# Kernel tuning notes

Hardware: AMD Instinct MI355X
Metric: run time of the kernel (lower is better)

Reference implementation:

```python
import jax, jax.numpy as jnp
import numpy as np
from jax import lax

# dims
B, N, D, H, K, NS = 16, 4096, 64, 128, 32, 1024  # clouds, pts/cloud, feat, hidden, max neighbors, fps samples
R = 0.2  # radius


def _fps(pos, n_s):
    """Farthest point sampling on one cloud. pos: [N,3] -> idx [n_s] int32."""
    n = pos.shape[0]

    def step(carry, _):
        dist, last = carry
        d = jnp.sum((pos - pos[last]) ** 2, axis=-1)
        dist = jnp.minimum(dist, d)
        nxt = jnp.argmax(dist).astype(jnp.int32)
        return (dist, nxt), last

    init = (jnp.full((n,), 1e10, pos.dtype), jnp.int32(0))
    _, idx = lax.scan(step, init, None, length=n_s)
    return idx


def setup_inputs() -> dict:
    key = jax.random.key(0)
    ks = jax.random.split(key, 6)
    s1 = 1.0 / np.sqrt(D + 1)
    s2 = 1.0 / np.sqrt(H)
    s3 = 1.0 / np.sqrt(D + H)
    return {
        "x": jax.random.normal(ks[0], (B, N, D), jnp.float32),
        "pos": jax.random.uniform(ks[1], (B, N, 3), jnp.float32),
        "W1": jax.random.normal(ks[2], (D + 1, H), jnp.float32) * s1,
        "b1": jnp.zeros((H,), jnp.float32),
        "W2": jax.random.normal(ks[3], (H, 3), jnp.float32) * s2,
        "b2": jnp.zeros((3,), jnp.float32),
        "W3": jax.random.normal(ks[4], (D + H, H), jnp.float32) * s3,
        "b3": jnp.zeros((H,), jnp.float32),
    }


def reference(x, pos, W1, b1, W2, b2, W3, b3):
    # 1) FPS downsample per cloud -> centers
    idx = jax.vmap(lambda p: _fps(p, NS))(pos)                    # [B,NS]
    pos_s = jax.vmap(lambda p, i: p[i])(pos, idx)                 # [B,NS,3]

    # 2) radius neighbor search: nearest-K within R (<= max_num_neighbors=32)
    d2 = jnp.sum((pos_s[:, :, None, :] - pos[:, None, :, :]) ** 2, axis=-1)  # [B,NS,N]
    masked = jnp.where(d2 <= R * R, d2, jnp.inf)
    neg, nbr = lax.top_k(-masked, K)                              # nearest K
    valid = (-neg) <= R * R                                       # [B,NS,K]

    # 3) gather neighbor features/positions
    x_j = jax.vmap(lambda a, i: a[i])(x, nbr)                     # [B,NS,K,D]
    pos_j = jax.vmap(lambda a, i: a[i])(pos, nbr)                 # [B,NS,K,3]
    diff = pos_j - pos_s[:, :, None, :]                           # pos_j - pos_i
    d2sel = jnp.sum(diff ** 2, axis=-1)
    dist = jnp.where(d2sel > 0, jnp.sqrt(jnp.where(d2sel > 0, d2sel, 1.0)), 0.0)

    # 4) message MLPs
    feat = jnp.concatenate([x_j, dist[..., None]], axis=-1)       # [B,NS,K,D+1]
    emb = jax.nn.relu(feat @ W1 + b1)                             # nn_msg_x
    pw = emb @ W2 + b2                                            # nn_msg_pos
    pmsg = diff * pw

    # 5) masked aggregate: sum for x, mean for pos
    m = valid[..., None].astype(emb.dtype)
    aggr_x = jnp.sum(emb * m, axis=2)                             # [B,NS,H]
    cnt = jnp.maximum(jnp.sum(m, axis=2), 1.0)                    # [B,NS,1]
    aggr_pos = jnp.sum(pmsg * m, axis=2) / cnt                    # [B,NS,3]

    # 6) update
    x_d = jax.vmap(lambda a, i: a[i])(x, idx)                     # [B,NS,D]
    out_x = jax.nn.relu(jnp.concatenate([x_d, aggr_x], axis=-1) @ W3 + b3)
    out_pos = pos_s + aggr_pos
    return out_x, out_pos, idx
```

## Files before the change

### kernel.cpp

```cpp
#include <hip/hip_runtime.h>
#include <math.h>

#define B_ 16
#define N_ 4096
#define D_ 64
#define H_ 128
#define K_ 32
#define NS_ 1024
#define R2_ 0.04f
#define CAP_ 1024

typedef short short8 __attribute__((ext_vector_type(8)));
typedef float f32x4 __attribute__((ext_vector_type(4)));

static __device__ __forceinline__ short f2bf(float f) {
    unsigned u = __float_as_uint(f);
    unsigned r = (u + 0x7FFFu + ((u >> 16) & 1u)) >> 16;
    return (short)r;
}

template<int CTRL, int RM>
static __device__ __forceinline__ unsigned dppmov(unsigned v) {
    return (unsigned)__builtin_amdgcn_update_dpp((int)v, (int)v, CTRL, RM, 0xF, false);
}

#define DPP_FMAX_STEP(CTRL, RM)                                           \
    {                                                                     \
        float n = __uint_as_float(dppmov<CTRL, RM>(__float_as_uint(wm))); \
        wm = fmaxf(wm, n);                                                \
    }

#define DPP_UMIN_STEP(CTRL, RM)                                           \
    {                                                                     \
        unsigned n = dppmov<CTRL, RM>(cand);                              \
        cand = n < cand ? n : cand;                                       \
    }

#define DPP_UMIN_STEP_V(var, CTRL, RM)                                    \
    {                                                                     \
        unsigned n = dppmov<CTRL, RM>(var);                               \
        var = n < var ? n : var;                                          \
    }

__global__ __launch_bounds__(256, 1) void mega_kernel(
    const float* __restrict__ pos, const float* __restrict__ x,
    const float* __restrict__ W1, const float* __restrict__ b1,
    const float* __restrict__ W2, const float* __restrict__ b2,
    const float* __restrict__ W3, const float* __restrict__ b3,
    int* ticket, int* progress, int* idx_i, float* pos_s,
    float* out_x, float* out_pos, float* idx_f)
{
    __shared__ __align__(16) char smem[66048];
    __shared__ int srole;
    const int t = threadIdx.x;
    if (t == 0) srole = atomicAdd(ticket, 1);
    __syncthreads();
    const int my = srole;
    const int wv = t >> 6;
    const int lane = t & 63;

    if (my < B_) {
        float4* lpos4 = (float4*)smem;
        unsigned long long (*skey)[4] = (unsigned long long (*)[4])(smem + 65536);
        float4 (*scoord)[4] = (float4 (*)[4])(smem + 65536 + 64);
        const int b = my;
        const float* posb = pos + (size_t)b * N_ * 3;
        for (int p = t; p < N_; p += 256)
            lpos4[p] = make_float4(posb[3 * p + 0], posb[3 * p + 1], posb[3 * p + 2], 0.f);
        __syncthreads();

        float px[16], py[16], pz[16], dist[16];
#pragma unroll
        for (int j = 0; j < 16; ++j) {
            float4 v = lpos4[t + 256 * j];
            px[j] = v.x; py[j] = v.y; pz[j] = v.z;
            dist[j] = 1e10f;
        }
        unsigned curidx = 0;
        float4 c0 = lpos4[0];
        float ccx = c0.x, ccy = c0.y, ccz = c0.z;

        for (int ns = 0; ns < NS_; ++ns) {
            if (t == 0) {
                idx_i[b * NS_ + ns] = (int)curidx;
                idx_f[b * NS_ + ns] = (float)curidx;
                pos_s[(b * NS_ + ns) * 3 + 0] = ccx;
                pos_s[(b * NS_ + ns) * 3 + 1] = ccy;
                pos_s[(b * NS_ + ns) * 3 + 2] = ccz;
            }
            float bv = -1.f; int bj = 0;
#pragma unroll
            for (int j = 0; j < 16; ++j) {
                float dx = __fsub_rn(px[j], ccx);
                float dy = __fsub_rn(py[j], ccy);
                float dz = __fsub_rn(pz[j], ccz);
                float d2 = __fadd_rn(__fadd_rn(__fmul_rn(dx, dx), __fmul_rn(dy, dy)), __fmul_rn(dz, dz));
                float dn = fminf(dist[j], d2);
                dist[j] = dn;
                bool g = dn > bv;
                bv = g ? dn : bv;
                bj = g ? j : bj;
            }
            float wm = bv;
            DPP_FMAX_STEP(0x111, 0xF)
            DPP_FMAX_STEP(0x112, 0xF)
            DPP_FMAX_STEP(0x114, 0xF)
            DPP_FMAX_STEP(0x118, 0xF)
            DPP_FMAX_STEP(0x142, 0xA)
            DPP_FMAX_STEP(0x143, 0xC)
            const float wavemax = __uint_as_float(
                (unsigned)__builtin_amdgcn_readlane((int)__float_as_uint(wm), 63));
            const unsigned pidx = (unsigned)t + ((unsigned)bj << 8);
            const unsigned long long mask = __ballot(bv == wavemax);
            unsigned widx;
            if (__popcll(mask) == 1) {
                const int wl = __ffsll((long long)mask) - 1;
                widx = (unsigned)__builtin_amdgcn_readlane((int)pidx, wl);
            } else {
                unsigned cand = (bv == wavemax) ? pidx : 0xFFFFFFFFu;
                DPP_UMIN_STEP(0x111, 0xF)
                DPP_UMIN_STEP(0x112, 0xF)
                DPP_UMIN_STEP(0x114, 0xF)
                DPP_UMIN_STEP(0x118, 0xF)
                DPP_UMIN_STEP(0x142, 0xA)
                DPP_UMIN_STEP(0x143, 0xC)
                widx = (unsigned)__builtin_amdgcn_readlane((int)cand, 63);
            }
            float4 wc = lpos4[widx];
            if (lane == 0) {
                skey[ns & 1][wv] = (((unsigned long long)__float_as_uint(wavemax)) << 32)
                                 | (unsigned long long)(0xFFFFFFFFu - widx);
                scoord[ns & 1][wv] = wc;
            }
            __syncthreads();
            {
                unsigned sid = (unsigned)(lane & 3);
                unsigned long long skv = skey[ns & 1][sid];
                float4 scv = scoord[ns & 1][sid];
                unsigned kh2 = (unsigned)(skv >> 32), kl2 = (unsigned)skv;
#define SLOT_STEP(CTRL)                                                        \
                {                                                              \
                    unsigned nh = dppmov<CTRL, 0xF>(kh2);                      \
                    unsigned nl = dppmov<CTRL, 0xF>(kl2);                      \
                    unsigned nsid = dppmov<CTRL, 0xF>(sid);                    \
                    unsigned long long nk = (((unsigned long long)nh) << 32) | nl; \
                    unsigned long long ok = (((unsigned long long)kh2) << 32) | kl2;\
                    if (nk > ok) { kh2 = nh; kl2 = nl; sid = nsid; }           \
                }
                SLOT_STEP(0x101)
                SLOT_STEP(0x102)
#undef SLOT_STEP
                const int slotwin = __builtin_amdgcn_readfirstlane((int)sid);
                curidx = 0xFFFFFFFFu - (unsigned)__builtin_amdgcn_readfirstlane((int)kl2);
                ccx = __uint_as_float((unsigned)__builtin_amdgcn_readlane(
                          (int)__float_as_uint(scv.x), slotwin));
                ccy = __uint_as_float((unsigned)__builtin_amdgcn_readlane(
                          (int)__float_as_uint(scv.y), slotwin));
                ccz = __uint_as_float((unsigned)__builtin_amdgcn_readlane(
                          (int)__float_as_uint(scv.z), slotwin));
            }
            if (((ns & 63) == 63) && t == 0) {
                __threadfence();
                __hip_atomic_store(progress + b, ns + 1,
                                   __ATOMIC_RELEASE, __HIP_MEMORY_SCOPE_AGENT);
            }
        }
        return;
    }

    const int wt = my - B_;
    const int b = wt & 15;
    const int c = wt >> 4;
    const int s0 = b * NS_ + c * 16;
    const int quad = lane >> 4, cl = lane & 15;
    unsigned long long* ckw = (unsigned long long*)smem + (size_t)wv * CAP_;
    char* wbp = smem + 32768 + wv * 5120;
    float* rows = (float*)(smem + 53248);

    short8 bfrag[8][2];
    float b1v[8], w1dv[8], w2v0[8], w2v1[8], w2v2[8];
#pragma unroll
    for (int Nt = 0; Nt < 8; ++Nt) {
        const int h = Nt * 16 + cl;
#pragma unroll
        for (int ks = 0; ks < 2; ++ks) {
            short8 f;
#pragma unroll
            for (int jj = 0; jj < 8; ++jj)
                f[jj] = f2bf(W1[(ks * 32 + quad * 8 + jj) * H_ + h]);
            bfrag[Nt][ks] = f;
        }
        b1v[Nt] = b1[h];
        w1dv[Nt] = W1[64 * H_ + h];
        w2v0[Nt] = W2[h * 3 + 0];
        w2v1[Nt] = W2[h * 3 + 1];
        w2v2[Nt] = W2[h * 3 + 2];
    }
    const float b20 = b2[0], b21 = b2[1], b22 = b2[2];

    if (t == 0) {
        const int need = c * 16 + 16;
        while (__hip_atomic_load(progress + b, __ATOMIC_ACQUIRE,
                                 __HIP_MEMORY_SCOPE_AGENT) < need)
            __builtin_amdgcn_s_sleep(8);
    }
    __syncthreads();
    __threadfence();

    const volatile float* psv = pos_s;
    const volatile int*   iiv = idx_i;
    const float* posb = pos + (size_t)b * N_ * 3;
    const int kkg = lane >> 1, half = lane & 1;

    for (int i = 0; i < 4; ++i) {
        const int s = s0 + wv * 4 + i;
        const int sl = wv * 4 + i;
        const float cx = psv[s * 3 + 0], cy = psv[s * 3 + 1], cz = psv[s * 3 + 2];
        int m = 0;
        for (int base = 0; base < N_; base += 64) {
            int p = base + lane;
            float dx = __fsub_rn(posb[3 * p + 0], cx);
            float dy = __fsub_rn(posb[3 * p + 1], cy);
            float dz = __fsub_rn(posb[3 * p + 2], cz);
            float d2 = __fadd_rn(__fadd_rn(__fmul_rn(dx, dx), __fmul_rn(dy, dy)), __fmul_rn(dz, dz));
            bool in = (d2 <= R2_);
            unsigned long long msk = __ballot(in);
            int before = __popcll(msk & ((1ull << lane) - 1ull));
            int slot = m + before;
            if (in && slot < CAP_)
                ckw[slot] = ((unsigned long long)__float_as_uint(d2) << 32) | (unsigned)p;
            m += __popcll(msk);
        }
        if (m > CAP_) m = CAP_;
        __asm__ volatile("s_waitcnt lgkmcnt(0)" ::: "memory");
        const int kcnt = m < K_ ? m : K_;
        int nidx = -1;
        if (m <= 256) {
            unsigned long long kr[4];
#pragma unroll
            for (int r = 0; r < 4; ++r) {
                int q = r * 64 + lane;
                unsigned long long v = ckw[q & (CAP_ - 1)];
                kr[r] = (q < m) ? v : ~0ull;
            }
            unsigned chosen = 0;
            for (int k = 0; k < kcnt; ++k) {
                unsigned long long localk = ~0ull; int br = -1;
#pragma unroll
                for (int r = 0; r < 4; ++r) {
                    bool ok = (!((chosen >> r) & 1u)) && (kr[r] < localk);
                    localk = ok ? kr[r] : localk;
                    br = ok ? r : br;
                }
                const unsigned mybits = (unsigned)(localk >> 32);
                const unsigned myidx = (unsigned)localk;
                unsigned wb2 = mybits;
                DPP_UMIN_STEP_V(wb2, 0x111, 0xF)
                DPP_UMIN_STEP_V(wb2, 0x112, 0xF)
                DPP_UMIN_STEP_V(wb2, 0x114, 0xF)
                DPP_UMIN_STEP_V(wb2, 0x118, 0xF)
                DPP_UMIN_STEP_V(wb2, 0x142, 0xA)
                DPP_UMIN_STEP_V(wb2, 0x143, 0xC)
                const unsigned minbits = (unsigned)__builtin_amdgcn_readlane((int)wb2, 63);
                const unsigned long long wmask = __ballot(mybits == minbits);
                unsigned widx;
                if (__popcll(wmask) == 1) {
                    const int wl = __ffsll((long long)wmask) - 1;
                    widx = (unsigned)__builtin_amdgcn_readlane((int)myidx, wl);
                } else {
                    unsigned cand = (mybits == minbits) ? myidx : 0xFFFFFFFFu;
                    DPP_UMIN_STEP(0x111, 0xF)
                    DPP_UMIN_STEP(0x112, 0xF)
                    DPP_UMIN_STEP(0x114, 0xF)
                    DPP_UMIN_STEP(0x118, 0xF)
                    DPP_UMIN_STEP(0x142, 0xA)
                    DPP_UMIN_STEP(0x143, 0xC)
                    widx = (unsigned)__builtin_amdgcn_readlane((int)cand, 63);
                }
                if (mybits == minbits && myidx == widx) chosen |= 1u << br;
                if (kkg == k) nidx = (int)widx;
            }
        } else {
            unsigned chosen = 0;
            for (int k = 0; k < kcnt; ++k) {
                unsigned long long localk = ~0ull; int bslot = -1;
                for (int r = 0; r * 64 + lane < m; ++r) {
                    if (chosen & (1u << r)) continue;
                    int q = r * 64 + lane;
                    unsigned long long key = ckw[q];
                    if (key < localk) { localk = key; bslot = q; }
                }
                unsigned kh = (unsigned)(localk >> 32), kl = (unsigned)localk;
#define DPP_MIN_STEP2(CTRL, RM)                                               \
                {                                                             \
                    unsigned nh = dppmov<CTRL, RM>(kh);                       \
                    unsigned nl = dppmov<CTRL, RM>(kl);                       \
                    unsigned long long nk = (((unsigned long long)nh) << 32) | nl; \
                    unsigned long long ok = (((unsigned long long)kh) << 32) | kl; \
                    if (nk < ok) { kh = nh; kl = nl; }                        \
                }
                DPP_MIN_STEP2(0x111, 0xF)
                DPP_MIN_STEP2(0x112, 0xF)
                DPP_MIN_STEP2(0x114, 0xF)
                DPP_MIN_STEP2(0x118, 0xF)
                DPP_MIN_STEP2(0x142, 0xA)
                DPP_MIN_STEP2(0x143, 0xC)
#undef DPP_MIN_STEP2
                unsigned mh = (unsigned)__builtin_amdgcn_readlane((int)kh, 63);
                unsigned ml = (unsigned)__builtin_amdgcn_readlane((int)kl, 63);
                unsigned long long bk = (((unsigned long long)mh) << 32) | ml;
                if (localk == bk && bslot >= 0) chosen |= 1u << (bslot >> 6);
                if (kkg == k) nidx = (int)(bk & 0xFFFFFFFFull);
            }
        }
        const float cnt = (kcnt < 1) ? 1.f : (float)kcnt;
        {
            char* frow = wbp + kkg * 144 + half * 64;
            const int n = nidx;
            if (n >= 0) {
                const float4* xr = (const float4*)(x + ((size_t)b * N_ + n) * D_) + half * 8;
#pragma unroll
                for (int q = 0; q < 4; ++q) {
                    float4 a = xr[q * 2], cc = xr[q * 2 + 1];
                    short8 o;
                    o[0] = f2bf(a.x); o[1] = f2bf(a.y); o[2] = f2bf(a.z); o[3] = f2bf(a.w);
                    o[4] = f2bf(cc.x); o[5] = f2bf(cc.y); o[6] = f2bf(cc.z); o[7] = f2bf(cc.w);
                    *(short8*)(frow + q * 16) = o;
                }
            } else {
                short8 z = {0, 0, 0, 0, 0, 0, 0, 0};
#pragma unroll
                for (int q = 0; q < 4; ++q) *(short8*)(frow + q * 16) = z;
            }
            if (half == 0) {
                float dxm = 0.f, dym = 0.f, dzm = 0.f, de = -1.f;
                if (n >= 0) {
                    const float* pj = pos + ((size_t)b * N_ + n) * 3;
                    float dx = pj[0] - cx;
                    float dy = pj[1] - cy;
                    float dz = pj[2] - cz;
                    float d2 = dx * dx + dy * dy + dz * dz;
                    de = d2 > 0.f ? sqrtf(d2) : 0.f;
                    dxm = dx; dym = dy; dzm = dz;
                }
                f32x4 sv = {dxm, dym, dzm, de};
                *(f32x4*)(wbp + 4608 + kkg * 16) = sv;
            }
        }
        float agp[8] = {0, 0, 0, 0, 0, 0, 0, 0};
        float gp0[8] = {0, 0, 0, 0, 0, 0, 0, 0};
        float gp1[8] = {0, 0, 0, 0, 0, 0, 0, 0};
        float gp2[8] = {0, 0, 0, 0, 0, 0, 0, 0};
#pragma unroll
        for (int Mt = 0; Mt < 2; ++Mt) {
            short8 a0 = *(short8*)(wbp + (Mt * 16 + cl) * 144 + quad * 16);
            short8 a1 = *(short8*)(wbp + (Mt * 16 + cl) * 144 + 64 + quad * 16);
            f32x4 acc[8];
#pragma unroll
            for (int Nt = 0; Nt < 8; ++Nt) {
                f32x4 z = {0.f, 0.f, 0.f, 0.f};
                z = __builtin_amdgcn_mfma_f32_16x16x32_bf16(a0, bfrag[Nt][0], z, 0, 0, 0);
                z = __builtin_amdgcn_mfma_f32_16x16x32_bf16(a1, bfrag[Nt][1], z, 0, 0, 0);
                acc[Nt] = z;
            }
            f32x4 sd[4];
#pragma unroll
            for (int r = 0; r < 4; ++r)
                sd[r] = *(f32x4*)(wbp + 4608 + (Mt * 16 + quad * 4 + r) * 16);
#pragma unroll
            for (int Nt = 0; Nt < 8; ++Nt) {
#pragma unroll
                for (int r = 0; r < 4; ++r) {
                    float dr = sd[r][3];
                    float wgt = dr >= 0.f ? 1.f : 0.f;
                    float dd = dr >= 0.f ? dr : 0.f;
                    float e = fmaf(dd, w1dv[Nt], acc[Nt][r]) + b1v[Nt];
                    e = e > 0.f ? e : 0.f;
                    agp[Nt] = fmaf(wgt, e, agp[Nt]);
                    gp0[Nt] = fmaf(sd[r][0], e, gp0[Nt]);
                    gp1[Nt] = fmaf(sd[r][1], e, gp1[Nt]);
                    gp2[Nt] = fmaf(sd[r][2], e, gp2[Nt]);
                }
            }
        }
#pragma unroll
        for (int Nt = 0; Nt < 8; ++Nt) {
            float v = agp[Nt]; v += __shfl_xor(v, 16); v += __shfl_xor(v, 32);
            if (quad == 0) rows[sl * 200 + 64 + Nt * 16 + cl] = v;
            float g0 = gp0[Nt]; g0 += __shfl_xor(g0, 16); g0 += __shfl_xor(g0, 32); gp0[Nt] = g0;
            float g1 = gp1[Nt]; g1 += __shfl_xor(g1, 16); g1 += __shfl_xor(g1, 32); gp1[Nt] = g1;
            float g2 = gp2[Nt]; g2 += __shfl_xor(g2, 16); g2 += __shfl_xor(g2, 32); gp2[Nt] = g2;
        }
        float pr0 = 0.f, pr1 = 0.f, pr2 = 0.f;
#pragma unroll
        for (int Nt = 0; Nt < 8; ++Nt) {
            pr0 = fmaf(w2v0[Nt], gp0[Nt], pr0);
            pr1 = fmaf(w2v1[Nt], gp1[Nt], pr1);
            pr2 = fmaf(w2v2[Nt], gp2[Nt], pr2);
        }
#pragma unroll
        for (int off = 1; off < 16; off <<= 1) {
            pr0 += __shfl_xor(pr0, off);
            pr1 += __shfl_xor(pr1, off);
            pr2 += __shfl_xor(pr2, off);
        }
        f32x4 dsv = *(f32x4*)(wbp + 4608 + (lane & 31) * 16);
        float q0 = dsv[0], q1 = dsv[1], q2 = dsv[2];
#pragma unroll
        for (int off = 1; off < 32; off <<= 1) {
            q0 += __shfl_xor(q0, off);
            q1 += __shfl_xor(q1, off);
            q2 += __shfl_xor(q2, off);
        }
        if (lane < 3) {
            float pr = lane == 0 ? pr0 : (lane == 1 ? pr1 : pr2);
            float qq = lane == 0 ? q0 : (lane == 1 ? q1 : q2);
            float bb = lane == 0 ? b20 : (lane == 1 ? b21 : b22);
            out_pos[s * 3 + lane] = psv[s * 3 + lane] + (pr + bb * qq) / cnt;
        }
    }
    __syncthreads();
    {
        const int sl = t >> 4, part = t & 15;
        const int id = iiv[s0 + sl];
        const float4* xr = (const float4*)(x + ((size_t)b * N_ + id) * D_);
        *(float4*)&rows[sl * 200 + part * 4] = xr[part];
    }
    __syncthreads();
    {
        const int hhalf = t >> 7, h = t & 127;
        const int r0 = hhalf * 8;
        float acc[8];
#pragma unroll
        for (int r = 0; r < 8; ++r) acc[r] = 0.f;
        for (int j4 = 0; j4 < 48; ++j4) {
            float w0 = W3[(j4 * 4 + 0) * H_ + h];
            float w1 = W3[(j4 * 4 + 1) * H_ + h];
            float w2 = W3[(j4 * 4 + 2) * H_ + h];
            float w3 = W3[(j4 * 4 + 3) * H_ + h];
#pragma unroll
            for (int r = 0; r < 8; ++r) {
                const float4 f = *(const float4*)&rows[(r0 + r) * 200 + j4 * 4];
                float a = acc[r];
                a = fmaf(f.x, w0, a); a = fmaf(f.y, w1, a);
                a = fmaf(f.z, w2, a); a = fmaf(f.w, w3, a);
                acc[r] = a;
            }
        }
        const float bb = b3[h];
#pragma unroll
        for (int r = 0; r < 8; ++r) {
            float v = acc[r] + bb;
            v = v > 0.f ? v : 0.f;
            out_x[(size_t)(s0 + r0 + r) * H_ + h] = v;
        }
    }
}

extern "C" void kernel_launch(void* const* d_in, const int* in_sizes, int n_in,
                              void* d_out, int out_size, void* d_ws, size_t ws_size,
                              hipStream_t stream) {
    const float* x   = (const float*)d_in[0];
    const float* pos = (const float*)d_in[1];
    const float* W1  = (const float*)d_in[2];
    const float* b1  = (const float*)d_in[3];
    const float* W2  = (const float*)d_in[4];
    const float* b2  = (const float*)d_in[5];
    const float* W3  = (const float*)d_in[6];
    const float* b3  = (const float*)d_in[7];

    float* out_x   = (float*)d_out;
    float* out_pos = (float*)d_out + 2097152;
    float* idx_f   = (float*)d_out + 2146304;

    char* ws = (char*)d_ws;
    int*   ticket   = (int*)ws;
    int*   progress = (int*)(ws + 64);
    float* pos_s    = (float*)(ws + 1024);
    int*   idx_i    = (int*)(ws + 1024 + 196608);

    hipMemsetAsync(ws, 0, 256, stream);
    mega_kernel<<<B_ + 1024, 256, 0, stream>>>(pos, x, W1, b1, W2, b2, W3, b3,
                                               ticket, progress, idx_i, pos_s,
                                               out_x, out_pos, idx_f);
}
```

Measured before the change: 1.050 ms.

## Split persistent mega-kernel into separate FPS and worker kernel launches

Replaces the single ticket-based kernel, in which FPS blocks publish progress and worker blocks spin-wait on it, with two sequential launches: an FPS kernel over 16 blocks and a worker kernel over 1024 blocks. FPS results are buffered in shared memory and written out once at the end, rather than by thread 0 on every iteration. This removes the memset, the atomics, the spin-waits and the volatile reads. The cost is that the neighbour/MLP work no longer overlaps the long serial FPS phase.

Measured after the change: 1.162 ms. +10.7%, slower.

```diff
diff --git a/kernel.cpp b/kernel.cpp
--- a/kernel.cpp
+++ b/kernel.cpp
@@ -42,137 +42,136 @@
         var = n < var ? n : var;                                          \
     }
 
-__global__ __launch_bounds__(256, 1) void mega_kernel(
+__global__ __launch_bounds__(256, 1) void fps_kernel(
+    const float* __restrict__ pos, int* __restrict__ idx_i,
+    float* __restrict__ idx_f, float* __restrict__ pos_s)
+{
+    __shared__ float4 lpos4[N_];
+    __shared__ float4 sres[NS_];
+    __shared__ unsigned long long skey[2][4];
+    __shared__ float4 scoord[2][4];
+    const int b = blockIdx.x;
+    const int t = threadIdx.x;
+    const int wv = t >> 6;
+    const int lane = t & 63;
+    const float* posb = pos + (size_t)b * N_ * 3;
+    for (int p = t; p < N_; p += 256)
+        lpos4[p] = make_float4(posb[3 * p + 0], posb[3 * p + 1], posb[3 * p + 2], 0.f);
+    __syncthreads();
+
+    float px[16], py[16], pz[16], dist[16];
+#pragma unroll
+    for (int j = 0; j < 16; ++j) {
+        float4 v = lpos4[t + 256 * j];
+        px[j] = v.x; py[j] = v.y; pz[j] = v.z;
+        dist[j] = 1e10f;
+    }
+    unsigned curidx = 0;
+    float4 c0 = lpos4[0];
+    float ccx = c0.x, ccy = c0.y, ccz = c0.z;
+
+    for (int ns = 0; ns < NS_; ++ns) {
+        if (t == 0)
+            sres[ns] = make_float4(ccx, ccy, ccz, __uint_as_float(curidx));
+        float bv = -1.f; int bj = 0;
+#pragma unroll
+        for (int j = 0; j < 16; ++j) {
+            float dx = __fsub_rn(px[j], ccx);
+            float dy = __fsub_rn(py[j], ccy);
+            float dz = __fsub_rn(pz[j], ccz);
+            float d2 = __fadd_rn(__fadd_rn(__fmul_rn(dx, dx), __fmul_rn(dy, dy)), __fmul_rn(dz, dz));
+            float dn = fminf(dist[j], d2);
+            dist[j] = dn;
+            bool g = dn > bv;
+            bv = g ? dn : bv;
+            bj = g ? j : bj;
+        }
+        float wm = bv;
+        DPP_FMAX_STEP(0x111, 0xF)
+        DPP_FMAX_STEP(0x112, 0xF)
+        DPP_FMAX_STEP(0x114, 0xF)
+        DPP_FMAX_STEP(0x118, 0xF)
+        DPP_FMAX_STEP(0x142, 0xA)
+        DPP_FMAX_STEP(0x143, 0xC)
+        const float wavemax = __uint_as_float(
+            (unsigned)__builtin_amdgcn_readlane((int)__float_as_uint(wm), 63));
+        const unsigned pidx = (unsigned)t + ((unsigned)bj << 8);
+        const unsigned long long mask = __ballot(bv == wavemax);
+        unsigned widx;
+        if (__popcll(mask) == 1) {
+            const int wl = __ffsll((long long)mask) - 1;
+            widx = (unsigned)__builtin_amdgcn_readlane((int)pidx, wl);
+        } else {
+            unsigned cand = (bv == wavemax) ? pidx : 0xFFFFFFFFu;
+            DPP_UMIN_STEP(0x111, 0xF)
+            DPP_UMIN_STEP(0x112, 0xF)
+            DPP_UMIN_STEP(0x114, 0xF)
+            DPP_UMIN_STEP(0x118, 0xF)
+            DPP_UMIN_STEP(0x142, 0xA)
+            DPP_UMIN_STEP(0x143, 0xC)
+            widx = (unsigned)__builtin_amdgcn_readlane((int)cand, 63);
+        }
+        float4 wc = lpos4[widx];
+        if (lane == 0) {
+            skey[ns & 1][wv] = (((unsigned long long)__float_as_uint(wavemax)) << 32)
+                             | (unsigned long long)(0xFFFFFFFFu - widx);
+            scoord[ns & 1][wv] = wc;
+        }
+        __syncthreads();
+        {
+            unsigned sid = (unsigned)(lane & 3);
+            unsigned long long skv = skey[ns & 1][sid];
+            float4 scv = scoord[ns & 1][sid];
+            unsigned kh2 = (unsigned)(skv >> 32), kl2 = (unsigned)skv;
+#define SLOT_STEP(CTRL)                                                        \
+            {                                                                  \
+                unsigned nh = dppmov<CTRL, 0xF>(kh2);                          \
+                unsigned nl = dppmov<CTRL, 0xF>(kl2);                          \
+                unsigned nsid = dppmov<CTRL, 0xF>(sid);                        \
+                unsigned long long nk = (((unsigned long long)nh) << 32) | nl; \
+                unsigned long long ok = (((unsigned long long)kh2) << 32) | kl2;\
+                if (nk > ok) { kh2 = nh; kl2 = nl; sid = nsid; }               \
+            }
+            SLOT_STEP(0x101)
+            SLOT_STEP(0x102)
+#undef SLOT_STEP
+            const int slotwin = __builtin_amdgcn_readfirstlane((int)sid);
+            curidx = 0xFFFFFFFFu - (unsigned)__builtin_amdgcn_readfirstlane((int)kl2);
+            ccx = __uint_as_float((unsigned)__builtin_amdgcn_readlane(
+                      (int)__float_as_uint(scv.x), slotwin));
+            ccy = __uint_as_float((unsigned)__builtin_amdgcn_readlane(
+                      (int)__float_as_uint(scv.y), slotwin));
+            ccz = __uint_as_float((unsigned)__builtin_amdgcn_readlane(
+                      (int)__float_as_uint(scv.z), slotwin));
+        }
+    }
+    __syncthreads();
+    for (int i = t; i < NS_; i += 256) {
+        float4 r = sres[i];
+        unsigned id = __float_as_uint(r.w);
+        idx_i[b * NS_ + i] = (int)id;
+        idx_f[b * NS_ + i] = (float)id;
+        pos_s[(b * NS_ + i) * 3 + 0] = r.x;
+        pos_s[(b * NS_ + i) * 3 + 1] = r.y;
+        pos_s[(b * NS_ + i) * 3 + 2] = r.z;
+    }
+}
+
+__global__ __launch_bounds__(256, 1) void worker_kernel(
     const float* __restrict__ pos, const float* __restrict__ x,
     const float* __restrict__ W1, const float* __restrict__ b1,
     const float* __restrict__ W2, const float* __restrict__ b2,
     const float* __restrict__ W3, const float* __restrict__ b3,
-    int* ticket, int* progress, int* idx_i, float* pos_s,
-    float* out_x, float* out_pos, float* idx_f)
+    const int* __restrict__ idx_i, const float* __restrict__ pos_s,
+    float* __restrict__ out_x, float* __restrict__ out_pos)
 {
     __shared__ __align__(16) char smem[66048];
-    __shared__ int srole;
     const int t = threadIdx.x;
-    if (t == 0) srole = atomicAdd(ticket, 1);
-    __syncthreads();
-    const int my = srole;
-    const int wv = t >> 6;
-    const int lane = t & 63;
-
-    if (my < B_) {
-        float4* lpos4 = (float4*)smem;
-        unsigned long long (*skey)[4] = (unsigned long long (*)[4])(smem + 65536);
-        float4 (*scoord)[4] = (float4 (*)[4])(smem + 65536 + 64);
-        const int b = my;
-        const float* posb = pos + (size_t)b * N_ * 3;
-        for (int p = t; p < N_; p += 256)
-            lpos4[p] = make_float4(posb[3 * p + 0], posb[3 * p + 1], posb[3 * p + 2], 0.f);
-        __syncthreads();
-
-        float px[16], py[16], pz[16], dist[16];
-#pragma unroll
-        for (int j = 0; j < 16; ++j) {
-            float4 v = lpos4[t + 256 * j];
-            px[j] = v.x; py[j] = v.y; pz[j] = v.z;
-            dist[j] = 1e10f;
-        }
-        unsigned curidx = 0;
-        float4 c0 = lpos4[0];
-        float ccx = c0.x, ccy = c0.y, ccz = c0.z;
-
-        for (int ns = 0; ns < NS_; ++ns) {
-            if (t == 0) {
-                idx_i[b * NS_ + ns] = (int)curidx;
-                idx_f[b * NS_ + ns] = (float)curidx;
-                pos_s[(b * NS_ + ns) * 3 + 0] = ccx;
-                pos_s[(b * NS_ + ns) * 3 + 1] = ccy;
-                pos_s[(b * NS_ + ns) * 3 + 2] = ccz;
-            }
-            float bv = -1.f; int bj = 0;
-#pragma unroll
-            for (int j = 0; j < 16; ++j) {
-                float dx = __fsub_rn(px[j], ccx);
-                float dy = __fsub_rn(py[j], ccy);
-                float dz = __fsub_rn(pz[j], ccz);
-                float d2 = __fadd_rn(__fadd_rn(__fmul_rn(dx, dx), __fmul_rn(dy, dy)), __fmul_rn(dz, dz));
-                float dn = fminf(dist[j], d2);
-                dist[j] = dn;
-                bool g = dn > bv;
-                bv = g ? dn : bv;
-                bj = g ? j : bj;
-            }
-            float wm = bv;
-            DPP_FMAX_STEP(0x111, 0xF)
-            DPP_FMAX_STEP(0x112, 0xF)
-            DPP_FMAX_STEP(0x114, 0xF)
-            DPP_FMAX_STEP(0x118, 0xF)
-            DPP_FMAX_STEP(0x142, 0xA)
-            DPP_FMAX_STEP(0x143, 0xC)
-            const float wavemax = __uint_as_float(
-                (unsigned)__builtin_amdgcn_readlane((int)__float_as_uint(wm), 63));
-            const unsigned pidx = (unsigned)t + ((unsigned)bj << 8);
-            const unsigned long long mask = __ballot(bv == wavemax);
-            unsigned widx;
-            if (__popcll(mask) == 1) {
-                const int wl = __ffsll((long long)mask) - 1;
-                widx = (unsigned)__builtin_amdgcn_readlane((int)pidx, wl);
-            } else {
-                unsigned cand = (bv == wavemax) ? pidx : 0xFFFFFFFFu;
-                DPP_UMIN_STEP(0x111, 0xF)
-                DPP_UMIN_STEP(0x112, 0xF)
-                DPP_UMIN_STEP(0x114, 0xF)
-                DPP_UMIN_STEP(0x118, 0xF)
-                DPP_UMIN_STEP(0x142, 0xA)
-                DPP_UMIN_STEP(0x143, 0xC)
-                widx = (unsigned)__builtin_amdgcn_readlane((int)cand, 63);
-            }
-            float4 wc = lpos4[widx];
-            if (lane == 0) {
-                skey[ns & 1][wv] = (((unsigned long long)__float_as_uint(wavemax)) << 32)
-                                 | (unsigned long long)(0xFFFFFFFFu - widx);
-                scoord[ns & 1][wv] = wc;
-            }
-            __syncthreads();
-            {
-                unsigned sid = (unsigned)(lane & 3);
-                unsigned long long skv = skey[ns & 1][sid];
-                float4 scv = scoord[ns & 1][sid];
-                unsigned kh2 = (unsigned)(skv >> 32), kl2 = (unsigned)skv;
-#define SLOT_STEP(CTRL)                                                        \
-                {                                                              \
-                    unsigned nh = dppmov<CTRL, 0xF>(kh2);                      \
-                    unsigned nl = dppmov<CTRL, 0xF>(kl2);                      \
-                    unsigned nsid = dppmov<CTRL, 0xF>(sid);                    \
-                    unsigned long long nk = (((unsigned long long)nh) << 32) | nl; \
-                    unsigned long long ok = (((unsigned long long)kh2) << 32) | kl2;\
-                    if (nk > ok) { kh2 = nh; kl2 = nl; sid = nsid; }           \
-                }
-                SLOT_STEP(0x101)
-                SLOT_STEP(0x102)
-#undef SLOT_STEP
-                const int slotwin = __builtin_amdgcn_readfirstlane((int)sid);
-                curidx = 0xFFFFFFFFu - (unsigned)__builtin_amdgcn_readfirstlane((int)kl2);
-                ccx = __uint_as_float((unsigned)__builtin_amdgcn_readlane(
-                          (int)__float_as_uint(scv.x), slotwin));
-                ccy = __uint_as_float((unsigned)__builtin_amdgcn_readlane(
-                          (int)__float_as_uint(scv.y), slotwin));
-                ccz = __uint_as_float((unsigned)__builtin_amdgcn_readlane(
-                          (int)__float_as_uint(scv.z), slotwin));
-            }
-            if (((ns & 63) == 63) && t == 0) {
-                __threadfence();
-                __hip_atomic_store(progress + b, ns + 1,
-                                   __ATOMIC_RELEASE, __HIP_MEMORY_SCOPE_AGENT);
-            }
-        }
-        return;
-    }
-
-    const int wt = my - B_;
-    const int b = wt & 15;
-    const int c = wt >> 4;
+    const int wv = t >> 6, lane = t & 63;
+    const int quad = lane >> 4, cl = lane & 15;
+    const int b = blockIdx.x >> 6;
+    const int c = blockIdx.x & 63;
     const int s0 = b * NS_ + c * 16;
-    const int quad = lane >> 4, cl = lane & 15;
     unsigned long long* ckw = (unsigned long long*)smem + (size_t)wv * CAP_;
     char* wbp = smem + 32768 + wv * 5120;
     float* rows = (float*)(smem + 53248);
@@ -198,24 +197,13 @@
     }
     const float b20 = b2[0], b21 = b2[1], b22 = b2[2];
 
-    if (t == 0) {
-        const int need = c * 16 + 16;
-        while (__hip_atomic_load(progress + b, __ATOMIC_ACQUIRE,
-                                 __HIP_MEMORY_SCOPE_AGENT) < need)
-            __builtin_amdgcn_s_sleep(8);
-    }
-    __syncthreads();
-    __threadfence();
-
-    const volatile float* psv = pos_s;
-    const volatile int*   iiv = idx_i;
     const float* posb = pos + (size_t)b * N_ * 3;
     const int kkg = lane >> 1, half = lane & 1;
 
     for (int i = 0; i < 4; ++i) {
         const int s = s0 + wv * 4 + i;
         const int sl = wv * 4 + i;
-        const float cx = psv[s * 3 + 0], cy = psv[s * 3 + 1], cz = psv[s * 3 + 2];
+        const float cx = pos_s[s * 3 + 0], cy = pos_s[s * 3 + 1], cz = pos_s[s * 3 + 2];
         int m = 0;
         for (int base = 0; base < N_; base += 64) {
             int p = base + lane;
@@ -416,13 +404,13 @@
             float pr = lane == 0 ? pr0 : (lane == 1 ? pr1 : pr2);
             float qq = lane == 0 ? q0 : (lane == 1 ? q1 : q2);
             float bb = lane == 0 ? b20 : (lane == 1 ? b21 : b22);
-            out_pos[s * 3 + lane] = psv[s * 3 + lane] + (pr + bb * qq) / cnt;
+            out_pos[s * 3 + lane] = pos_s[s * 3 + lane] + (pr + bb * qq) / cnt;
         }
     }
     __syncthreads();
     {
         const int sl = t >> 4, part = t & 15;
-        const int id = iiv[s0 + sl];
+        const int id = idx_i[s0 + sl];
         const float4* xr = (const float4*)(x + ((size_t)b * N_ + id) * D_);
         *(float4*)&rows[sl * 200 + part * 4] = xr[part];
     }
@@ -474,13 +462,10 @@
     float* idx_f   = (float*)d_out + 2146304;
 
     char* ws = (char*)d_ws;
-    int*   ticket   = (int*)ws;
-    int*   progress = (int*)(ws + 64);
-    float* pos_s    = (float*)(ws + 1024);
-    int*   idx_i    = (int*)(ws + 1024 + 196608);
-
-    hipMemsetAsync(ws, 0, 256, stream);
-    mega_kernel<<<B_ + 1024, 256, 0, stream>>>(pos, x, W1, b1, W2, b2, W3, b3,
-                                               ticket, progress, idx_i, pos_s,
-                                               out_x, out_pos, idx_f);
+    int*   idx_i = (int*)ws;
+    float* pos_s = (float*)(ws + 65536);
+
+    fps_kernel<<<B_, 256, 0, stream>>>(pos, idx_i, idx_f, pos_s);
+    worker_kernel<<<B_ * 64, 256, 0, stream>>>(pos, x, W1, b1, W2, b2, W3, b3,
+                                               idx_i, pos_s, out_x, out_pos);
 }
```
